# Performance work log

Measured on AMD Instinct MI355X. Metric: run time of the kernel, lower is better.

Reference implementation:

```python
import jax, jax.numpy as jnp
import numpy as np

N = 100000          # original nodes
E = 1600000         # edges (avg degree 16)
D_IN = 128
D_BLOOM = 16        # (bloom_lmax+1)^2 with lmax=3
D_OUT = 128
D_INTER = D_BLOOM + D_OUT
K = 4               # blooms per node
PF = 4              # pool factor (nodes per cluster)
C = N // PF         # coarsened nodes
MIN_RADIUS = 0.1


def setup_inputs() -> dict:
    key = jax.random.key(0)
    ks = jax.random.split(key, 10)
    x = jax.random.normal(ks[0], (N, D_IN), jnp.float32)
    pos = jax.random.normal(ks[1], (N, 3), jnp.float32)
    edge_index = jax.random.randint(ks[2], (2, E), 0, N)
    edge_attr = jax.random.normal(ks[3], (E, 3), jnp.float32)
    batch = jnp.sort(jax.random.randint(ks[4], (N,), 0, 64))
    # learned parameters (stand-ins for the injected submodules)
    W_conv = jax.random.normal(ks[5], (D_IN, D_INTER), jnp.float32) / np.sqrt(D_IN)
    W_edge = jax.random.normal(ks[6], (3, D_INTER), jnp.float32)
    D_bloom = jax.random.normal(ks[7], (K, D_BLOOM, 3), jnp.float32) / np.sqrt(D_BLOOM)
    W_gather = jax.random.normal(ks[8], (D_OUT, D_OUT), jnp.float32) / np.sqrt(D_OUT)
    W_gattr = jax.random.normal(ks[9], (3, D_OUT), jnp.float32)
    return dict(x=x, pos=pos, edge_index=edge_index, edge_attr=edge_attr, batch=batch,
                W_conv=W_conv, W_edge=W_edge, D_bloom=D_bloom,
                W_gather=W_gather, W_gattr=W_gattr)


def reference(x, pos, edge_index, edge_attr, batch, W_conv, W_edge, D_bloom, W_gather, W_gattr):
    src, dst = edge_index[0], edge_index[1]

    # ---- bloom conv: per-edge message, scatter-sum to destination nodes ----
    msg = x[src] @ W_conv + edge_attr @ W_edge           # [E, D_INTER]
    out = jax.ops.segment_sum(msg, dst, num_segments=N)  # [N, D_INTER]
    sph = out[:, :D_BLOOM]                               # [N, D_BLOOM]
    feat = out[:, D_BLOOM:]                              # [N, D_OUT]

    # ---- bloom: K candidate points per node ----
    offsets = MIN_RADIUS * jnp.tanh(jnp.einsum('nb,kbd->nkd', sph, D_bloom))  # [N,K,3]
    bloom_pos = (pos[:, None, :] + offsets).reshape(N * K, 3)
    bloom_batch = jnp.repeat(jnp.arange(N), K)           # bloom node -> original node

    # ---- cluster: deterministic pool_factor grouping ----
    clusters = bloom_batch // PF                         # [N*K] bloom -> cluster
    node_cluster = jnp.arange(N) // PF                   # [N] node -> cluster (coalesced pairs)

    # new_pos = scatter_mean(pos[coalesced node], cluster): exactly PF nodes per cluster
    new_pos = jax.ops.segment_sum(pos, node_cluster, num_segments=C) / PF  # [C,3]

    # ---- gather conv: bipartite message passing N features -> C clusters ----
    gather_edge_attr = pos[bloom_batch] - new_pos[clusters]                 # [N*K,3]
    gm = feat[bloom_batch] @ W_gather + gather_edge_attr @ W_gattr          # [N*K,D_OUT]
    x_new = jax.ops.segment_sum(gm, clusters, num_segments=C) / (K * PF)    # [C,D_OUT]

    # ---- new_edge_index: spspmm chain == map endpoints to clusters + coalesce ----
    enc = node_cluster[src] * C + node_cluster[dst]      # encode cluster pairs
    enc_u = jnp.unique(enc, size=E, fill_value=0)        # coalesced, padded with (0,0)
    new_edge_index = jnp.stack([enc_u // C, enc_u % C])  # [2, E] (padded)
    new_edge_attr = new_pos[new_edge_index[1]] - new_pos[new_edge_index[0]]

    # ---- new_batch: graph id of each cluster (batch is sorted per graph) ----
    new_batch = jax.ops.segment_max(batch, node_cluster, num_segments=C)

    return (x_new, new_pos, new_edge_index, new_edge_attr, new_batch)
```

## Files before the change

### kernel.cpp

```cpp
#include <hip/hip_runtime.h>
#include <hip/hip_bf16.h>
#include <stdint.h>

typedef unsigned int uint_t;
typedef unsigned short ushort_t;

#define NN 100000
#define EE 1600000
#define CC 25000
#define DINTER 144
#define NBKT 196
#define NBKT2 1568
#define NSEG 6272
#define KCAP 1024

#define W_M1B      0u
#define W_AGGB     8384u
#define W_PAGG     1658384u
#define W_PKA4     14858384u
#define W_PKC      21258384u
#define W_OFFS2    22858384u
#define W_BHA2     23058385u
#define W_BHC      23059953u
#define W_BBA2     23060149u
#define W_BCURA2   23061718u
#define W_BBC      23063286u
#define W_BCURC    23063483u
#define WS_WORDS   23066816u

#define O_XNEW  0u
#define O_POS   3200000u
#define O_EI    3275000u
#define O_ATTR  6475000u
#define O_BATCH 11275000u

static __device__ __forceinline__ uint_t f2bf(float f) {
    union { float f; uint_t i; } v; v.f = f;
    uint_t x = v.i;
    return (x + 0x7fffu + ((x >> 16) & 1u)) >> 16;
}
static __device__ __forceinline__ float bf2f(ushort_t u) {
    union { uint_t i; float f; } v; v.i = ((uint_t)u) << 16; return v.f;
}

__global__ void xpack(const float4* __restrict__ x4, uint2* __restrict__ xb2) {
    int i = blockIdx.x * 256 + threadIdx.x;
    if (i >= NN * 32) return;
    float4 v = x4[i];
    uint2 r;
    r.x = f2bf(v.x) | (f2bf(v.y) << 16);
    r.y = f2bf(v.z) | (f2bf(v.w) << 16);
    xb2[i] = r;
}

__global__ void build_m1f(const float* __restrict__ Wconv,
                          const float* __restrict__ Wedge,
                          const float* __restrict__ Wg,
                          ushort_t* __restrict__ m1b) {
    int j = blockIdx.x;
    int o = threadIdx.x;
    const float* wrow = (j < 128) ? (Wconv + j * DINTER + 16)
                                  : (Wedge + (j - 128) * DINTER + 16);
    float acc = 0.f;
    for (int f = 0; f < 128; ++f)
        acc += wrow[f] * Wg[f * 128 + o];
    m1b[j * 128 + o] = (ushort_t)f2bf(acc);
}

__global__ void edge_hist2(const int* __restrict__ ei,
                           uint_t* __restrict__ bhA2, uint_t* __restrict__ bhC) {
    __shared__ uint_t hA[NBKT2], hC[NBKT];
    int tid = threadIdx.x;
    for (int i = tid; i < NBKT2; i += 1024) hA[i] = 0;
    for (int i = tid; i < NBKT; i += 1024) hC[i] = 0;
    __syncthreads();
    for (int e = blockIdx.x * 1024 + tid; e < EE; e += 256 * 1024) {
        uint_t u = (uint_t)ei[e];
        uint_t v = (uint_t)ei[EE + e];
        atomicAdd(&hA[(u / 12500u) * 196u + (v >> 9)], 1u);
        atomicAdd(&hC[u >> 9], 1u);
    }
    __syncthreads();
    for (int i = tid; i < NBKT2; i += 1024) if (hA[i]) atomicAdd(&bhA2[i], hA[i]);
    for (int i = tid; i < NBKT; i += 1024)  if (hC[i]) atomicAdd(&bhC[i], hC[i]);
}

__global__ void scan_small(const uint_t* __restrict__ in, uint_t* __restrict__ out,
                           uint_t* __restrict__ out2, int n) {
    __shared__ uint_t part[256];
    int tid = threadIdx.x;
    int per = (n + 255) >> 8;
    int lo = tid * per;
    int hi = lo + per; if (hi > n) hi = n;
    if (lo > n) lo = n;
    uint_t s = 0;
    for (int i = lo; i < hi; ++i) s += in[i];
    part[tid] = s;
    __syncthreads();
    for (int off = 1; off < 256; off <<= 1) {
        uint_t v = (tid >= off) ? part[tid - off] : 0u;
        __syncthreads();
        part[tid] += v;
        __syncthreads();
    }
    uint_t run = part[tid] - s;
    for (int i = lo; i < hi; ++i) {
        out[i] = run;
        if (out2) out2[i] = run;
        run += in[i];
    }
    if (tid == 255) out[n] = run;
}

#define TPB 4096
__global__ void bucket_place_A2(const int* __restrict__ ei, const float* __restrict__ ea,
                                uint_t* __restrict__ bcur, uint4* __restrict__ pk4) {
    __shared__ uint_t hist[NBKT2], gbase[NBKT2], cur[NBKT2];
    int tid = threadIdx.x;
    int t0 = blockIdx.x * TPB;
    int nt = EE - t0; if (nt > TPB) nt = TPB;
    for (int i = tid; i < NBKT2; i += 1024) { hist[i] = 0; cur[i] = 0; }
    __syncthreads();
    for (int i = tid; i < nt; i += 1024) {
        int e = t0 + i;
        uint_t u = (uint_t)ei[e];
        uint_t v = (uint_t)ei[EE + e];
        atomicAdd(&hist[(u / 12500u) * 196u + (v >> 9)], 1u);
    }
    __syncthreads();
    for (int b = tid; b < NBKT2; b += 1024) {
        uint_t h = hist[b];
        if (h) gbase[b] = atomicAdd(&bcur[b], h);
    }
    __syncthreads();
    for (int i = tid; i < nt; i += 1024) {
        int e = t0 + i;
        uint_t u = (uint_t)ei[e];
        uint_t v = (uint_t)ei[EE + e];
        uint_t b = (u / 12500u) * 196u + (v >> 9);
        uint_t r = gbase[b] + atomicAdd(&cur[b], 1u);
        uint4 p;
        p.x = (((v >> 2) & 127u) << 17) | u;
        p.y = __float_as_uint(ea[(size_t)e * 3 + 0]);
        p.z = __float_as_uint(ea[(size_t)e * 3 + 1]);
        p.w = __float_as_uint(ea[(size_t)e * 3 + 2]);
        pk4[r] = p;
    }
}

__global__ void bucket_place_C(const int* __restrict__ ei, uint_t* __restrict__ bcur,
                               uint_t* __restrict__ pkC) {
    __shared__ uint_t pk[TPB];
    __shared__ uint_t gpk[TPB];
    __shared__ uint_t hist[NBKT], lbase[NBKT], gbase[NBKT], cur[NBKT];
    __shared__ uint_t part[1024];
    int tid = threadIdx.x;
    int t0 = blockIdx.x * TPB;
    int nt = EE - t0; if (nt > TPB) nt = TPB;
    for (int i = tid; i < NBKT; i += 1024) { hist[i] = 0; cur[i] = 0; }
    __syncthreads();
    for (int i = tid; i < nt; i += 1024) {
        int e = t0 + i;
        uint_t u = ((uint_t)ei[e]) >> 2;
        uint_t v = ((uint_t)ei[EE + e]) >> 2;
        uint_t w = (u << 15) | v;
        pk[i] = w;
        atomicAdd(&hist[w >> 22], 1u);
    }
    __syncthreads();
    uint_t h = (tid < NBKT) ? hist[tid] : 0u;
    if (tid < NBKT) gbase[tid] = atomicAdd(&bcur[tid], h);
    part[tid] = h;
    __syncthreads();
    for (int off = 1; off < 1024; off <<= 1) {
        uint_t v = (tid >= off) ? part[tid - off] : 0u;
        __syncthreads();
        part[tid] += v;
        __syncthreads();
    }
    if (tid < NBKT) lbase[tid] = part[tid] - h;
    __syncthreads();
    for (int i = tid; i < nt; i += 1024) {
        uint_t b = pk[i] >> 22;
        uint_t r = lbase[b] + atomicAdd(&cur[b], 1u);
        gpk[r] = pk[i];
    }
    __syncthreads();
    for (int r = tid; r < nt; r += 1024) {
        uint_t b = gpk[r] >> 22;
        pkC[gbase[b] + ((uint_t)r - lbase[b])] = gpk[r];
    }
}

__global__ void bucket_sort_A2(const uint_t* __restrict__ bbA2, const uint4* __restrict__ pk4,
                               uint_t* __restrict__ pkW, uint_t* __restrict__ paggw,
                               uint_t* __restrict__ offs2) {
    __shared__ uint4 st[2048];
    __shared__ uint_t hist[128], base2[128], cur[128];
    __shared__ float eacc0[128], eacc1[128], eacc2[128];
    __shared__ uint_t part[256];
    int tid = threadIdx.x, bk = blockIdx.x;
    uint_t s = bbA2[bk], epos = bbA2[bk + 1];
    int n = (int)(epos - s);
    if (n > 2048) n = 2048;
    if (tid < 128) {
        hist[tid] = 0; cur[tid] = 0;
        eacc0[tid] = 0.f; eacc1[tid] = 0.f; eacc2[tid] = 0.f;
    }
    for (int i = tid; i < n; i += 256) st[i] = pk4[s + i];
    __syncthreads();
    for (int i = tid; i < n; i += 256) {
        uint4 p = st[i];
        uint_t d = p.x >> 17;
        atomicAdd(&hist[d], 1u);
        atomicAdd(&eacc0[d], __uint_as_float(p.y));
        atomicAdd(&eacc1[d], __uint_as_float(p.z));
        atomicAdd(&eacc2[d], __uint_as_float(p.w));
    }
    __syncthreads();
    uint_t h = (tid < 128) ? hist[tid] : 0u;
    part[tid] = h;
    __syncthreads();
    for (int off = 1; off < 256; off <<= 1) {
        uint_t v = (tid >= off) ? part[tid - off] : 0u;
        __syncthreads();
        part[tid] += v;
        __syncthreads();
    }
    int sl = bk / 196, q = bk - sl * 196;
    if (tid < 128) {
        base2[tid] = part[tid] - h;
        int c = q * 128 + tid;
        if (c < CC) {
            uint_t kk = (uint_t)sl * CC + (uint_t)c;
            offs2[kk] = s + base2[tid];
            paggw[(size_t)kk * 66 + 64] = f2bf(eacc0[tid]) | (f2bf(eacc1[tid]) << 16);
            paggw[(size_t)kk * 66 + 65] = f2bf(eacc2[tid]);
        }
    }
    if (bk == 0 && tid == 0) offs2[8 * CC] = EE;
    __syncthreads();
    for (int i = tid; i < n; i += 256) {
        uint4 p = st[i];
        uint_t d = p.x >> 17;
        uint_t r = base2[d] + atomicAdd(&cur[d], 1u);
        pkW[s + r] = p.x;
    }
}

__global__ void bucket_sort_C(const uint_t* __restrict__ bbC, uint_t* __restrict__ pkC,
                              uint_t* __restrict__ csub) {
    __shared__ uint_t st[8960];
    __shared__ uint_t hist[32], base2[32], cur[32];
    __shared__ uint_t part[256];
    int tid = threadIdx.x, bk = blockIdx.x;
    uint_t s = bbC[bk], epos = bbC[bk + 1];
    int n = (int)(epos - s);
    if (n > 8960) n = 8960;
    if (tid < 32) { hist[tid] = 0; cur[tid] = 0; }
    for (int i = tid; i < n; i += 256) st[i] = pkC[s + i];
    __syncthreads();
    for (int i = tid; i < n; i += 256) atomicAdd(&hist[(st[i] >> 17) & 31u], 1u);
    __syncthreads();
    uint_t h = (tid < 32) ? hist[tid] : 0u;
    part[tid] = h;
    __syncthreads();
    for (int off = 1; off < 256; off <<= 1) {
        uint_t v = (tid >= off) ? part[tid - off] : 0u;
        __syncthreads();
        part[tid] += v;
        __syncthreads();
    }
    if (tid < 32) {
        base2[tid] = part[tid] - h;
        csub[bk * 32 + tid] = s + base2[tid];
    }
    if (bk == 0 && tid == 0) csub[NSEG] = EE;
    __syncthreads();
    for (int i = tid; i < n; i += 256) {
        uint_t w = st[i];
        uint_t d = (w >> 17) & 31u;
        uint_t r = base2[d] + atomicAdd(&cur[d], 1u);
        pkC[s + r] = w;
    }
}

__global__ void cluster_pass(const float* __restrict__ pos, const int* __restrict__ batch,
                             float* __restrict__ out) {
    int c = blockIdx.x * 256 + threadIdx.x;
    if (c >= CC) return;
    float px = 0.f, py = 0.f, pz = 0.f;
    for (int j = 0; j < 4; ++j) {
        int n = c * 4 + j;
        px += pos[n * 3 + 0];
        py += pos[n * 3 + 1];
        pz += pos[n * 3 + 2];
    }
    px *= 0.25f; py *= 0.25f; pz *= 0.25f;
    out[O_POS + c * 3 + 0] = px;
    out[O_POS + c * 3 + 1] = py;
    out[O_POS + c * 3 + 2] = pz;
    int b = batch[c * 4];
    b = max(b, batch[c * 4 + 1]);
    b = max(b, batch[c * 4 + 2]);
    b = max(b, batch[c * 4 + 3]);
    out[O_BATCH + c] = (float)b;
}

__global__ void cluster_reduce4(const uint_t* __restrict__ offs2, const uint_t* __restrict__ pkW,
                                const uint_t* __restrict__ xb, uint_t* __restrict__ paggw) {
    int tid = threadIdx.x;
    int lane = tid & 63;
    int s = blockIdx.x & 7;
    int c = (blockIdx.x >> 3) * 4 + (tid >> 6);
    uint_t kk = (uint_t)s * CC + (uint_t)c;
    uint_t start = (uint_t)__builtin_amdgcn_readfirstlane((int)offs2[kk]);
    uint_t end   = (uint_t)__builtin_amdgcn_readfirstlane((int)offs2[kk + 1]);
    const uint_t* xl = xb + lane;
    float a0 = 0.f, a1 = 0.f;
    uint_t i = start;
    for (; i + 4u <= end; i += 4u) {
        uint_t w0 = pkW[i + 0u];
        uint_t w1 = pkW[i + 1u];
        uint_t w2 = pkW[i + 2u];
        uint_t w3 = pkW[i + 3u];
        uint_t x0 = xl[(size_t)(w0 & 0x1FFFFu) * 64u];
        uint_t x1 = xl[(size_t)(w1 & 0x1FFFFu) * 64u];
        uint_t x2 = xl[(size_t)(w2 & 0x1FFFFu) * 64u];
        uint_t x3 = xl[(size_t)(w3 & 0x1FFFFu) * 64u];
        a0 += bf2f((ushort_t)(x0 & 0xffffu)); a1 += bf2f((ushort_t)(x0 >> 16));
        a0 += bf2f((ushort_t)(x1 & 0xffffu)); a1 += bf2f((ushort_t)(x1 >> 16));
        a0 += bf2f((ushort_t)(x2 & 0xffffu)); a1 += bf2f((ushort_t)(x2 >> 16));
        a0 += bf2f((ushort_t)(x3 & 0xffffu)); a1 += bf2f((ushort_t)(x3 >> 16));
    }
    for (; i < end; ++i) {
        uint_t wj = pkW[i];
        uint_t xv = xl[(size_t)(wj & 0x1FFFFu) * 64u];
        a0 += bf2f((ushort_t)(xv & 0xffffu));
        a1 += bf2f((ushort_t)(xv >> 16));
    }
    paggw[(size_t)kk * 66 + lane] = f2bf(a0) | (f2bf(a1) << 16);
}

__global__ void agg_merge(const uint_t* __restrict__ paggw, uint_t* __restrict__ aggw) {
    int j = blockIdx.x * 256 + threadIdx.x;
    if (j >= 1650000) return;
    float lo = 0.f, hi = 0.f;
    #pragma unroll
    for (int s = 0; s < 8; ++s) {
        uint_t w = paggw[(size_t)s * 1650000u + (uint_t)j];
        lo += bf2f((ushort_t)(w & 0xffffu));
        hi += bf2f((ushort_t)(w >> 16));
    }
    aggw[j] = f2bf(lo) | (f2bf(hi) << 16);
}

#define GEMM_CPB 32
__global__ void gemm_tiled(const ushort_t* __restrict__ aggb, const ushort_t* __restrict__ m1b,
                           float* __restrict__ out) {
    __shared__ ushort_t m1s[131 * 128];
    __shared__ __align__(16) float srowT[132][8];
    int tid = threadIdx.x;
    {
        const uint_t* m1w = (const uint_t*)m1b;
        uint_t* m1sw = (uint_t*)m1s;
        for (int i = tid; i < 131 * 64; i += 256) m1sw[i] = m1w[i];
    }
    int o = tid & 127, half = tid >> 7;
    int c0b = blockIdx.x * GEMM_CPB;
    const uint_t* aggw = (const uint_t*)aggb;
    for (int it = 0; it < GEMM_CPB / 8; ++it) {
        int c0 = c0b + it * 8;
        __syncthreads();
        for (int i = tid; i < 528; i += 256) {
            int cg = i / 66, rem = i - cg * 66;
            int c = c0 + cg;
            uint_t w = (c < CC) ? aggw[(size_t)c * 66 + rem] : 0u;
            srowT[rem * 2][cg]     = bf2f((ushort_t)(w & 0xffffu));
            srowT[rem * 2 + 1][cg] = bf2f((ushort_t)(w >> 16));
        }
        __syncthreads();
        float acc0 = 0.f, acc1 = 0.f, acc2 = 0.f, acc3 = 0.f;
        #pragma unroll 4
        for (int j = 0; j < 131; ++j) {
            float m = bf2f(m1s[j * 128 + o]);
            float4 s = *(const float4*)&srowT[j][half * 4];
            acc0 += s.x * m;
            acc1 += s.y * m;
            acc2 += s.z * m;
            acc3 += s.w * m;
        }
        int cb = c0 + half * 4;
        if (cb + 0 < CC) out[O_XNEW + (size_t)(cb + 0) * 128 + o] = 0.25f * acc0;
        if (cb + 1 < CC) out[O_XNEW + (size_t)(cb + 1) * 128 + o] = 0.25f * acc1;
        if (cb + 2 < CC) out[O_XNEW + (size_t)(cb + 2) * 128 + o] = 0.25f * acc2;
        if (cb + 3 < CC) out[O_XNEW + (size_t)(cb + 3) * 128 + o] = 0.25f * acc3;
    }
}

__global__ void enc_count(const uint_t* __restrict__ csub, const uint_t* __restrict__ pkC,
                          uint_t* __restrict__ bcnt, uint_t* __restrict__ kbuf) {
    __shared__ uint_t bmp[3125];
    __shared__ uint_t sh[256];
    int tid = threadIdx.x, bid = blockIdx.x;
    uint_t s = csub[bid], epos = csub[bid + 1];
    int n = (int)(epos - s);
    for (int i = tid; i < 3125; i += 256) bmp[i] = 0;
    __syncthreads();
    for (int i = tid; i < n; i += 256) {
        uint_t w = pkC[s + i];
        uint_t le = ((w >> 15) & 3u) * 25000u + (w & 32767u);
        atomicOr(&bmp[le >> 5], 1u << (le & 31u));
    }
    __syncthreads();
    int lo = tid * 13, hi = lo + 13;
    if (lo > 3125) lo = 3125;
    if (hi > 3125) hi = 3125;
    uint_t mine = 0;
    for (int i = lo; i < hi; ++i) mine += __popc(bmp[i]);
    sh[tid] = mine;
    __syncthreads();
    for (int off = 1; off < 256; off <<= 1) {
        uint_t v = (tid >= off) ? sh[tid - off] : 0u;
        __syncthreads();
        sh[tid] += v;
        __syncthreads();
    }
    uint_t r = sh[tid] - mine;
    uint_t kb = (uint_t)bid * KCAP;
    for (int i = lo; i < hi; ++i) {
        uint_t bits = bmp[i];
        while (bits) {
            int b = __builtin_ctz(bits);
            bits &= bits - 1u;
            if (r < KCAP) kbuf[kb + r] = (uint_t)i * 32u + (uint_t)b;
            r++;
        }
    }
    if (tid == 255) bcnt[bid] = min(sh[255], (uint_t)KCAP);
}

__global__ void enc_emit(const uint_t* __restrict__ ebase, const uint_t* __restrict__ kbuf,
                         float* __restrict__ out) {
    int tid = threadIdx.x, bid = blockIdx.x;
    uint_t g0 = ebase[bid], g1 = ebase[bid + 1];
    int cnt = (int)(g1 - g0);
    const float* np = out + O_POS;
    uint_t ubase = ((uint_t)(bid >> 5)) * 128u + ((uint_t)(bid & 31)) * 4u;
    uint_t kb = (uint_t)bid * KCAP;
    for (int r = tid; r < cnt; r += 256) {
        uint_t le = kbuf[kb + r];
        uint_t uo = le / 25000u;
        uint_t v = le - uo * 25000u;
        uint_t u = ubase + uo;
        uint_t rank = g0 + (uint_t)r;
        out[O_EI + rank] = (float)u;
        out[O_EI + EE + rank] = (float)v;
        out[O_ATTR + (size_t)rank * 3 + 0] = np[v * 3 + 0] - np[u * 3 + 0];
        out[O_ATTR + (size_t)rank * 3 + 1] = np[v * 3 + 1] - np[u * 3 + 1];
        out[O_ATTR + (size_t)rank * 3 + 2] = np[v * 3 + 2] - np[u * 3 + 2];
    }
}

extern "C" void kernel_launch(void* const* d_in, const int* in_sizes, int n_in,
                              void* d_out, int out_size, void* d_ws, size_t ws_size,
                              hipStream_t stream) {
    const float* x     = (const float*)d_in[0];
    const float* pos   = (const float*)d_in[1];
    const int*   ei    = (const int*)d_in[2];
    const float* ea    = (const float*)d_in[3];
    const int*   batch = (const int*)d_in[4];
    const float* Wconv = (const float*)d_in[5];
    const float* Wedge = (const float*)d_in[6];
    const float* Wg    = (const float*)d_in[8];

    float*  out = (float*)d_out;
    uint_t* ws  = (uint_t*)d_ws;

    if (ws_size < (size_t)WS_WORDS * 4) return;

    ushort_t* m1b    = (ushort_t*)(ws + W_M1B);
    ushort_t* aggb   = (ushort_t*)(ws + W_AGGB);
    uint_t*   pkW    = ws + W_AGGB;
    uint_t*   paggw  = ws + W_PAGG;
    uint4*    pk4    = (uint4*)(ws + W_PKA4);
    uint_t*   pkC    = ws + W_PKC;
    uint_t*   offs2  = ws + W_OFFS2;
    uint_t*   bhA2   = ws + W_BHA2;
    uint_t*   bhC    = ws + W_BHC;
    uint_t*   bbA2   = ws + W_BBA2;
    uint_t*   bcurA2 = ws + W_BCURA2;
    uint_t*   bbC    = ws + W_BBC;
    uint_t*   bcurC  = ws + W_BCURC;
    uint_t*   xb     = (uint_t*)(out + O_EI);
    uint_t*   csub   = ws + W_PKA4;
    uint_t*   bcnt2  = ws + W_PKA4 + 8192u;
    uint_t*   ebase2 = ws + W_PKA4 + 16384u;
    uint_t*   kbuf   = ws + W_PAGG;

    hipMemsetAsync(bhA2, 0, (size_t)(NBKT2 + NBKT) * 4, stream);

    xpack<<<dim3(12500), dim3(256), 0, stream>>>((const float4*)x, (uint2*)xb);
    build_m1f<<<dim3(131), dim3(128), 0, stream>>>(Wconv, Wedge, Wg, m1b);
    edge_hist2<<<dim3(256), dim3(1024), 0, stream>>>(ei, bhA2, bhC);
    scan_small<<<dim3(1), dim3(256), 0, stream>>>(bhA2, bbA2, bcurA2, NBKT2);
    scan_small<<<dim3(1), dim3(256), 0, stream>>>(bhC, bbC, bcurC, NBKT);
    bucket_place_A2<<<dim3((EE + TPB - 1) / TPB), dim3(1024), 0, stream>>>(ei, ea, bcurA2, pk4);
    bucket_place_C<<<dim3((EE + TPB - 1) / TPB), dim3(1024), 0, stream>>>(ei, bcurC, pkC);
    bucket_sort_A2<<<dim3(NBKT2), dim3(256), 0, stream>>>(bbA2, pk4, pkW, paggw, offs2);
    cluster_pass<<<dim3(98), dim3(256), 0, stream>>>(pos, batch, out);
    cluster_reduce4<<<dim3(50000), dim3(256), 0, stream>>>(offs2, pkW, xb, paggw);
    agg_merge<<<dim3(6446), dim3(256), 0, stream>>>(paggw, (uint_t*)aggb);
    gemm_tiled<<<dim3((CC + GEMM_CPB - 1) / GEMM_CPB), dim3(256), 0, stream>>>(aggb, m1b, out);
    hipMemsetAsync((char*)d_out + (size_t)O_EI * 4, 0, (size_t)(3200000 + 4800000) * 4, stream);
    bucket_sort_C<<<dim3(NBKT), dim3(256), 0, stream>>>(bbC, pkC, csub);
    enc_count<<<dim3(NSEG), dim3(256), 0, stream>>>(csub, pkC, bcnt2, kbuf);
    scan_small<<<dim3(1), dim3(256), 0, stream>>>(bcnt2, ebase2, (uint_t*)0, NSEG);
    enc_emit<<<dim3(NSEG), dim3(256), 0, stream>>>(ebase2, kbuf, out);
}
```

Measured before the change: 454.6 us.

## Fuse bucket placement kernels and fold partial-aggregate merge into GEMM

```diff
diff --git a/kernel.cpp b/kernel.cpp
--- a/kernel.cpp
+++ b/kernel.cpp
@@ -113,82 +113,70 @@
 }
 
 #define TPB 4096
-__global__ void bucket_place_A2(const int* __restrict__ ei, const float* __restrict__ ea,
-                                uint_t* __restrict__ bcur, uint4* __restrict__ pk4) {
-    __shared__ uint_t hist[NBKT2], gbase[NBKT2], cur[NBKT2];
+__global__ void bucket_place_AC(const int* __restrict__ ei, const float* __restrict__ ea,
+                                uint_t* __restrict__ bcurA, uint_t* __restrict__ bcurC,
+                                uint4* __restrict__ pk4, uint_t* __restrict__ pkC) {
+    __shared__ uint_t histA[NBKT2], gbaseA[NBKT2], curA[NBKT2];
+    __shared__ uint_t pkst[TPB];
+    __shared__ uint_t gpk[TPB];
+    __shared__ uint_t histC[NBKT], lbaseC[NBKT], gbaseC[NBKT], curC[NBKT];
+    __shared__ uint_t part[1024];
     int tid = threadIdx.x;
     int t0 = blockIdx.x * TPB;
     int nt = EE - t0; if (nt > TPB) nt = TPB;
-    for (int i = tid; i < NBKT2; i += 1024) { hist[i] = 0; cur[i] = 0; }
+    for (int i = tid; i < NBKT2; i += 1024) { histA[i] = 0; curA[i] = 0; }
+    for (int i = tid; i < NBKT; i += 1024) { histC[i] = 0; curC[i] = 0; }
     __syncthreads();
     for (int i = tid; i < nt; i += 1024) {
         int e = t0 + i;
         uint_t u = (uint_t)ei[e];
         uint_t v = (uint_t)ei[EE + e];
-        atomicAdd(&hist[(u / 12500u) * 196u + (v >> 9)], 1u);
+        atomicAdd(&histA[(u / 12500u) * 196u + (v >> 9)], 1u);
+        uint_t w = ((u >> 2) << 15) | (v >> 2);
+        pkst[i] = w;
+        atomicAdd(&histC[w >> 22], 1u);
     }
     __syncthreads();
     for (int b = tid; b < NBKT2; b += 1024) {
-        uint_t h = hist[b];
-        if (h) gbase[b] = atomicAdd(&bcur[b], h);
-    }
-    __syncthreads();
+        uint_t h = histA[b];
+        if (h) gbaseA[b] = atomicAdd(&bcurA[b], h);
+    }
+    uint_t h = (tid < NBKT) ? histC[tid] : 0u;
+    if (tid < NBKT) gbaseC[tid] = atomicAdd(&bcurC[tid], h);
+    part[tid] = h;
+    __syncthreads();
+    for (int off = 1; off < 1024; off <<= 1) {
+        uint_t v = (tid >= off) ? part[tid - off] : 0u;
+        __syncthreads();
+        part[tid] += v;
+        __syncthreads();
+    }
+    if (tid < NBKT) lbaseC[tid] = part[tid] - h;
+    __syncthreads();
+    for (int i = tid; i < nt; i += 1024) {
+        uint_t w = pkst[i];
+        uint_t b = w >> 22;
+        uint_t r = lbaseC[b] + atomicAdd(&curC[b], 1u);
+        gpk[r] = w;
+    }
+    __syncthreads();
+    for (int r = tid; r < nt; r += 1024) {
+        uint_t w = gpk[r];
+        uint_t b = w >> 22;
+        pkC[gbaseC[b] + ((uint_t)r - lbaseC[b])] = w;
+    }
     for (int i = tid; i < nt; i += 1024) {
         int e = t0 + i;
         uint_t u = (uint_t)ei[e];
         uint_t v = (uint_t)ei[EE + e];
         uint_t b = (u / 12500u) * 196u + (v >> 9);
-        uint_t r = gbase[b] + atomicAdd(&cur[b], 1u);
+        uint_t r = gbaseA[b] + atomicAdd(&curA[b], 1u);
         uint4 p;
         p.x = (((v >> 2) & 127u) << 17) | u;
         p.y = __float_as_uint(ea[(size_t)e * 3 + 0]);
         p.z = __float_as_uint(ea[(size_t)e * 3 + 1]);
         p.w = __float_as_uint(ea[(size_t)e * 3 + 2]);
         pk4[r] = p;
-    }
-}
-
-__global__ void bucket_place_C(const int* __restrict__ ei, uint_t* __restrict__ bcur,
-                               uint_t* __restrict__ pkC) {
-    __shared__ uint_t pk[TPB];
-    __shared__ uint_t gpk[TPB];
-    __shared__ uint_t hist[NBKT], lbase[NBKT], gbase[NBKT], cur[NBKT];
-    __shared__ uint_t part[1024];
-    int tid = threadIdx.x;
-    int t0 = blockIdx.x * TPB;
-    int nt = EE - t0; if (nt > TPB) nt = TPB;
-    for (int i = tid; i < NBKT; i += 1024) { hist[i] = 0; cur[i] = 0; }
-    __syncthreads();
-    for (int i = tid; i < nt; i += 1024) {
-        int e = t0 + i;
-        uint_t u = ((uint_t)ei[e]) >> 2;
-        uint_t v = ((uint_t)ei[EE + e]) >> 2;
-        uint_t w = (u << 15) | v;
-        pk[i] = w;
-        atomicAdd(&hist[w >> 22], 1u);
-    }
-    __syncthreads();
-    uint_t h = (tid < NBKT) ? hist[tid] : 0u;
-    if (tid < NBKT) gbase[tid] = atomicAdd(&bcur[tid], h);
-    part[tid] = h;
-    __syncthreads();
-    for (int off = 1; off < 1024; off <<= 1) {
-        uint_t v = (tid >= off) ? part[tid - off] : 0u;
-        __syncthreads();
-        part[tid] += v;
-        __syncthreads();
-    }
-    if (tid < NBKT) lbase[tid] = part[tid] - h;
-    __syncthreads();
-    for (int i = tid; i < nt; i += 1024) {
-        uint_t b = pk[i] >> 22;
-        uint_t r = lbase[b] + atomicAdd(&cur[b], 1u);
-        gpk[r] = pk[i];
-    }
-    __syncthreads();
-    for (int r = tid; r < nt; r += 1024) {
-        uint_t b = gpk[r] >> 22;
-        pkC[gbase[b] + ((uint_t)r - lbase[b])] = gpk[r];
     }
 }
 
@@ -342,21 +330,8 @@
     paggw[(size_t)kk * 66 + lane] = f2bf(a0) | (f2bf(a1) << 16);
 }
 
-__global__ void agg_merge(const uint_t* __restrict__ paggw, uint_t* __restrict__ aggw) {
-    int j = blockIdx.x * 256 + threadIdx.x;
-    if (j >= 1650000) return;
-    float lo = 0.f, hi = 0.f;
-    #pragma unroll
-    for (int s = 0; s < 8; ++s) {
-        uint_t w = paggw[(size_t)s * 1650000u + (uint_t)j];
-        lo += bf2f((ushort_t)(w & 0xffffu));
-        hi += bf2f((ushort_t)(w >> 16));
-    }
-    aggw[j] = f2bf(lo) | (f2bf(hi) << 16);
-}
-
 #define GEMM_CPB 32
-__global__ void gemm_tiled(const ushort_t* __restrict__ aggb, const ushort_t* __restrict__ m1b,
+__global__ void gemm_tiled(const uint_t* __restrict__ paggw, const ushort_t* __restrict__ m1b,
                            float* __restrict__ out) {
     __shared__ ushort_t m1s[131 * 128];
     __shared__ __align__(16) float srowT[132][8];
@@ -368,16 +343,23 @@
     }
     int o = tid & 127, half = tid >> 7;
     int c0b = blockIdx.x * GEMM_CPB;
-    const uint_t* aggw = (const uint_t*)aggb;
     for (int it = 0; it < GEMM_CPB / 8; ++it) {
         int c0 = c0b + it * 8;
         __syncthreads();
         for (int i = tid; i < 528; i += 256) {
             int cg = i / 66, rem = i - cg * 66;
             int c = c0 + cg;
-            uint_t w = (c < CC) ? aggw[(size_t)c * 66 + rem] : 0u;
-            srowT[rem * 2][cg]     = bf2f((ushort_t)(w & 0xffffu));
-            srowT[rem * 2 + 1][cg] = bf2f((ushort_t)(w >> 16));
+            float lo = 0.f, hi = 0.f;
+            if (c < CC) {
+                #pragma unroll
+                for (int s = 0; s < 8; ++s) {
+                    uint_t w = paggw[((size_t)s * 25000u + (uint_t)c) * 66 + rem];
+                    lo += bf2f((ushort_t)(w & 0xffffu));
+                    hi += bf2f((ushort_t)(w >> 16));
+                }
+            }
+            srowT[rem * 2][cg]     = lo;
+            srowT[rem * 2 + 1][cg] = hi;
         }
         __syncthreads();
         float acc0 = 0.f, acc1 = 0.f, acc2 = 0.f, acc3 = 0.f;
@@ -480,7 +462,6 @@
     if (ws_size < (size_t)WS_WORDS * 4) return;
 
     ushort_t* m1b    = (ushort_t*)(ws + W_M1B);
-    ushort_t* aggb   = (ushort_t*)(ws + W_AGGB);
     uint_t*   pkW    = ws + W_AGGB;
     uint_t*   paggw  = ws + W_PAGG;
     uint4*    pk4    = (uint4*)(ws + W_PKA4);
@@ -505,13 +486,11 @@
     edge_hist2<<<dim3(256), dim3(1024), 0, stream>>>(ei, bhA2, bhC);
     scan_small<<<dim3(1), dim3(256), 0, stream>>>(bhA2, bbA2, bcurA2, NBKT2);
     scan_small<<<dim3(1), dim3(256), 0, stream>>>(bhC, bbC, bcurC, NBKT);
-    bucket_place_A2<<<dim3((EE + TPB - 1) / TPB), dim3(1024), 0, stream>>>(ei, ea, bcurA2, pk4);
-    bucket_place_C<<<dim3((EE + TPB - 1) / TPB), dim3(1024), 0, stream>>>(ei, bcurC, pkC);
+    bucket_place_AC<<<dim3((EE + TPB - 1) / TPB), dim3(1024), 0, stream>>>(ei, ea, bcurA2, bcurC, pk4, pkC);
     bucket_sort_A2<<<dim3(NBKT2), dim3(256), 0, stream>>>(bbA2, pk4, pkW, paggw, offs2);
     cluster_pass<<<dim3(98), dim3(256), 0, stream>>>(pos, batch, out);
     cluster_reduce4<<<dim3(50000), dim3(256), 0, stream>>>(offs2, pkW, xb, paggw);
-    agg_merge<<<dim3(6446), dim3(256), 0, stream>>>(paggw, (uint_t*)aggb);
-    gemm_tiled<<<dim3((CC + GEMM_CPB - 1) / GEMM_CPB), dim3(256), 0, stream>>>(aggb, m1b, out);
+    gemm_tiled<<<dim3((CC + GEMM_CPB - 1) / GEMM_CPB), dim3(256), 0, stream>>>(paggw, m1b, out);
     hipMemsetAsync((char*)d_out + (size_t)O_EI * 4, 0, (size_t)(3200000 + 4800000) * 4, stream);
     bucket_sort_C<<<dim3(NBKT), dim3(256), 0, stream>>>(bbC, pkC, csub);
     enc_count<<<dim3(NSEG), dim3(256), 0, stream>>>(csub, pkC, bcnt2, kbuf);
```

New measurement: 431.6 us. 5.1% less time.
